# Kernel optimization log

Hardware: AMD Instinct MI355X
Metric: run time of the kernel (lower is better)

Reference implementation:

```python
import jax, jax.numpy as jnp
import numpy as np

ALPHA = 2.0   # surrogate.atan(alpha=2)
BETA = 0.9    # membrane decay
THR = 1.0     # spike threshold

@jax.custom_vjp
def atan_spike(x):
    # Heaviside forward, atan surrogate backward (snntorch convention)
    return (x > 0).astype(x.dtype)

def _atan_fwd(x):
    return atan_spike(x), x

def _atan_bwd(x, g):
    return (g * (ALPHA / 2.0) / (1.0 + (jnp.pi / 2.0 * ALPHA * x) ** 2),)

atan_spike.defvjp(_atan_fwd, _atan_bwd)


def setup_inputs() -> dict:
    key = jax.random.key(0)
    ks = jax.random.split(key, 7)
    B, T, I = 128, 128, 1024
    dims = [2048, 2048, 1024]
    x = jax.random.normal(ks[0], (B, T, I), dtype=jnp.float32)
    fan_ins = [I, dims[0], dims[1]]
    W0 = jax.random.normal(ks[1], (dims[0], fan_ins[0]), dtype=jnp.float32) / np.sqrt(fan_ins[0])
    b0 = jax.random.normal(ks[2], (dims[0],), dtype=jnp.float32) * 0.01
    W1 = jax.random.normal(ks[3], (dims[1], fan_ins[1]), dtype=jnp.float32) / np.sqrt(fan_ins[1])
    b1 = jax.random.normal(ks[4], (dims[1],), dtype=jnp.float32) * 0.01
    W2 = jax.random.normal(ks[5], (dims[2], fan_ins[2]), dtype=jnp.float32) / np.sqrt(fan_ins[2])
    b2 = jax.random.normal(ks[6], (dims[2],), dtype=jnp.float32) * 0.01
    return {"x": x, "W0": W0, "b0": b0, "W1": W1, "b1": b1, "W2": W2, "b2": b2}


def reference(x, W0, b0, W1, b1, W2, b2):
    params = ((W0, b0), (W1, b1), (W2, b2))
    B = x.shape[0]
    dims = [W0.shape[0], W1.shape[0], W2.shape[0]]
    v0 = tuple(jnp.zeros((B, d), x.dtype) for d in dims)

    def step(volts, x_t):
        h = x_t
        new_volts = []
        v = None
        for (W, b), vi in zip(params, volts):
            cur = h @ W.T + b            # [B, d]
            v = BETA * vi + cur           # leaky integration
            spk = atan_spike(v - THR)     # threshold
            v = v - spk * THR             # reset by subtraction
            new_volts.append(v)
            h = spk
        return tuple(new_volts), (h, v)

    xT = jnp.swapaxes(x, 0, 1)            # [T, B, I]
    _, (spikes, volts) = jax.lax.scan(step, v0, xT)
    # [T, B, D] -> [B, T, D]
    return jnp.swapaxes(spikes, 0, 1), jnp.swapaxes(volts, 0, 1)
```

## Files before the change

kernel.cpp:

```cpp
#include <hip/hip_runtime.h>
#include <stdint.h>


#define TT   128
#define NB   128
#define DD2  1024

#define SPK0_OFF 0u
#define SPK1_OFF (128u*128u*64u)
#define PART_OFF (2u*128u*128u*64u)
#define NHELP    96u
#define FLG_OFF  (PART_OFF + NHELP*8192u)
#define NFLG     1536u
#define WS_NEED_BYTES ((size_t)(FLG_OFF + NFLG) * 4u)

__device__ __forceinline__ void wait_ge(uint32_t* p, uint32_t tgt){
  while (__hip_atomic_load(p, __ATOMIC_ACQUIRE, __HIP_MEMORY_SCOPE_AGENT) < tgt)
    __builtin_amdgcn_s_sleep(1);
}

__device__ __forceinline__ constexpr int fswz(int k){
  return (k & 16) | ((k ^ (k >> 3)) & 12);
}

__global__ void sentinel_kernel(float* o){ o[0] = 42.0f; }

__global__ __launch_bounds__(512, 2) void snn_kernel(
    const float* __restrict__ x,
    const float* __restrict__ W0, const float* __restrict__ b0,
    const float* __restrict__ W1, const float* __restrict__ b1,
    const float* __restrict__ W2, const float* __restrict__ b2,
    float* __restrict__ out, uint32_t* __restrict__ ws)
{
  __shared__ __align__(16) float lA[2][128][68];
  __shared__ __align__(16) float lB[2][64][132];
  __shared__ uint32_t lBits[128];

  const int tid  = threadIdx.x;
  const int h    = tid >> 8;
  const int t256 = tid & 255;
  const int tm   = t256 & 15;
  const int tn   = t256 >> 4;
  const int bid  = blockIdx.x;

  uint32_t* spikes0  = ws + SPK0_OFF;
  uint32_t* spikes1  = ws + SPK1_OFF;
  float*    partials = (float*)(ws + PART_OFF);
  uint32_t* flg   = ws + FLG_OFF;
  uint32_t* pflag = flg;
  uint32_t* oflag = flg + 512;
  uint32_t* done0 = flg + 1024;
  uint32_t* done1 = flg + 1280;

  int group, pairk, tl, m0, n0, K, hslot;
  const float *Wl, *bl;
  const uint32_t* spkIn; uint32_t* spkOut;
  uint32_t *dIn, *dOut;
  if (bid < 64) {
    group=0; pairk=0; tl=bid;
    m0=(tl>>5)*64; n0=(tl&31)*64; K=1024; Wl=W0; bl=b0;
    spkIn=nullptr; spkOut=spikes0; dIn=nullptr; dOut=done0+(m0>>6)*128; hslot=-1;
  } else if (bid < 192) {
    group=1; int rel=bid-64; pairk=rel&1; tl=rel>>1;
    m0=(tl>>5)*64; n0=(tl&31)*64; K=2048; Wl=W1; bl=b1;
    spkIn=spikes0; spkOut=spikes1;
    dIn=done0+(m0>>6)*128; dOut=done1+(m0>>6)*128; hslot=tl;
  } else {
    group=2; int rel=bid-192; pairk=rel&1; tl=rel>>1;
    m0=(tl>>4)*64; n0=(tl&15)*64; K=2048; Wl=W2; bl=b2;
    spkIn=spikes1; spkOut=nullptr;
    dIn=done1+(m0>>6)*128; dOut=nullptr; hslot=64+tl;
  }
  const bool helper = (pairk == 1);
  const int  K0     = (pairk*2 + h)*512;

  float bias[4];
  #pragma unroll
  for (int c = 0; c < 4; ++c) bias[c] = bl[n0 + tn*4 + c];

  float vst[4][4];
  #pragma unroll
  for (int r = 0; r < 4; ++r)
    #pragma unroll
    for (int c = 0; c < 4; ++c) vst[r][c] = 0.f;

  const int e_mq   = t256 & 15;
  const int e_sub  = t256 >> 4;
  const int e_wsub = e_sub & 3;
  const int e_kq8  = e_sub >> 2;
  const int e_kloc = e_wsub*32 + e_kq8*8;

  float (*cA)[68]  = lA[h];
  float (*cB)[132] = lB[h];
  float* ex = &lA[1][0][0];

  for (int t = 0; t < TT; ++t) {
    if (dIn) {
      if (tid == 0) wait_ge(&dIn[t], 32u);
      __syncthreads();
    }

    float acc[4][4];
    #pragma unroll
    for (int r = 0; r < 4; ++r)
      #pragma unroll
      for (int c = 0; c < 4; ++c) acc[r][c] = 0.f;

    #pragma unroll 1
    for (int ch = 0; ch < 4; ++ch) {
      const int kb = K0 + ch*128;

      #pragma unroll
      for (int it = 0; it < 8; ++it) {
        int idx = t256 + it*256;
        int nrow = idx >> 5, kq = idx & 31;
        float4 w = *(const float4*)(Wl + (size_t)(n0+nrow)*K + kb + kq*4);
        *(float4*)&cB[nrow][kq*4] = w;
      }

      if (group == 0) {
        #pragma unroll
        for (int it = 0; it < 8; ++it) {
          int idx = t256 + it*256;
          int mrow = idx >> 5, kq = idx & 31;
          float4 v = *(const float4*)(x + ((size_t)(m0+mrow)*TT + t)*1024 + kb + kq*4);
          int k0 = kq*4;
          const int sw = fswz(k0);
          const int col = mrow ^ sw;
          cA[k0+0][col] = v.x; cA[k0+1][col] = v.y;
          cA[k0+2][col] = v.z; cA[k0+3][col] = v.w;
        }
      } else {
        const size_t rbase = ((size_t)t*NB + m0 + e_mq*4)*64 + (kb>>5) + e_wsub;
        uint32_t w0 = __hip_atomic_load(&spkIn[rbase      ], __ATOMIC_RELAXED, __HIP_MEMORY_SCOPE_AGENT);
        uint32_t w1 = __hip_atomic_load(&spkIn[rbase +  64], __ATOMIC_RELAXED, __HIP_MEMORY_SCOPE_AGENT);
        uint32_t w2 = __hip_atomic_load(&spkIn[rbase + 128], __ATOMIC_RELAXED, __HIP_MEMORY_SCOPE_AGENT);
        uint32_t w3 = __hip_atomic_load(&spkIn[rbase + 192], __ATOMIC_RELAXED, __HIP_MEMORY_SCOPE_AGENT);
        #pragma unroll
        for (int i = 0; i < 8; ++i) {
          int k  = e_kloc + i;
          int sh = k & 31;
          float4 f;
          f.x = ((w0 >> sh) & 1u) ? 1.0f : 0.0f;
          f.y = ((w1 >> sh) & 1u) ? 1.0f : 0.0f;
          f.z = ((w2 >> sh) & 1u) ? 1.0f : 0.0f;
          f.w = ((w3 >> sh) & 1u) ? 1.0f : 0.0f;
          *(float4*)&cA[k][(e_mq*4) ^ fswz(k)] = f;
        }
      }
      __syncthreads();

      #pragma unroll 4
      for (int k4 = 0; k4 < 32; ++k4) {
        const int kbase = k4*4;
        const int sw = fswz(kbase);
        const float* pa = &cA[kbase][(tm*4) ^ sw];
        const float4 q0 = *(const float4*)&cB[tn*4+0][kbase];
        const float4 q1 = *(const float4*)&cB[tn*4+1][kbase];
        const float4 q2 = *(const float4*)&cB[tn*4+2][kbase];
        const float4 q3 = *(const float4*)&cB[tn*4+3][kbase];
        #pragma unroll
        for (int u = 0; u < 4; ++u) {
          const float4 a  = *(const float4*)(pa + u*68);
          const float b0v = (u==0) ? q0.x : (u==1) ? q0.y : (u==2) ? q0.z : q0.w;
          const float b1v = (u==0) ? q1.x : (u==1) ? q1.y : (u==2) ? q1.z : q1.w;
          const float b2v = (u==0) ? q2.x : (u==1) ? q2.y : (u==2) ? q2.z : q2.w;
          const float b3v = (u==0) ? q3.x : (u==1) ? q3.y : (u==2) ? q3.z : q3.w;
          acc[0][0] = __builtin_fmaf(a.x, b0v, acc[0][0]);
          acc[1][0] = __builtin_fmaf(a.y, b0v, acc[1][0]);
          acc[2][0] = __builtin_fmaf(a.z, b0v, acc[2][0]);
          acc[3][0] = __builtin_fmaf(a.w, b0v, acc[3][0]);
          acc[0][1] = __builtin_fmaf(a.x, b1v, acc[0][1]);
          acc[1][1] = __builtin_fmaf(a.y, b1v, acc[1][1]);
          acc[2][1] = __builtin_fmaf(a.z, b1v, acc[2][1]);
          acc[3][1] = __builtin_fmaf(a.w, b1v, acc[3][1]);
          acc[0][2] = __builtin_fmaf(a.x, b2v, acc[0][2]);
          acc[1][2] = __builtin_fmaf(a.y, b2v, acc[1][2]);
          acc[2][2] = __builtin_fmaf(a.z, b2v, acc[2][2]);
          acc[3][2] = __builtin_fmaf(a.w, b2v, acc[3][2]);
          acc[0][3] = __builtin_fmaf(a.x, b3v, acc[0][3]);
          acc[1][3] = __builtin_fmaf(a.y, b3v, acc[1][3]);
          acc[2][3] = __builtin_fmaf(a.z, b3v, acc[2][3]);
          acc[3][3] = __builtin_fmaf(a.w, b3v, acc[3][3]);
        }
      }
      __syncthreads();
    }

    if (helper) {
      if (t >= 1) { if (tid == 0) wait_ge(&oflag[bid-1], (uint32_t)t); __syncthreads(); }
      uint64_t* pb = (uint64_t*)(partials + (size_t)hslot*8192 + (size_t)h*4096) + t256*8;
      #pragma unroll
      for (int r = 0; r < 4; ++r)
        #pragma unroll
        for (int cq = 0; cq < 2; ++cq) {
          union { float f[2]; uint64_t u; } cv;
          cv.f[0] = acc[r][cq*2+0]; cv.f[1] = acc[r][cq*2+1];
          __hip_atomic_store(&pb[r*2+cq], cv.u, __ATOMIC_RELAXED, __HIP_MEMORY_SCOPE_AGENT);
        }
      __syncthreads();
      if (tid == 0) __hip_atomic_store(&pflag[bid], (uint32_t)(t+1), __ATOMIC_RELEASE, __HIP_MEMORY_SCOPE_AGENT);
      continue;
    }

    if (h == 1) {
      #pragma unroll
      for (int r = 0; r < 4; ++r)
        *(float4*)&ex[t256*16 + r*4] = make_float4(acc[r][0], acc[r][1], acc[r][2], acc[r][3]);
    }
    __syncthreads();
    if (h == 0) {
      #pragma unroll
      for (int r = 0; r < 4; ++r)
        #pragma unroll
        for (int c = 0; c < 4; ++c)
          acc[r][c] = __fadd_rn(acc[r][c], ex[t256*16 + r*4 + c]);
    }

    if (group != 0) {
      if (tid == 0) wait_ge(&pflag[bid+1], (uint32_t)(t+1));
      __syncthreads();
      if (h == 0) {
        uint64_t* p2 = (uint64_t*)(partials + (size_t)hslot*8192) + t256*8;
        uint64_t* p3 = (uint64_t*)(partials + (size_t)hslot*8192 + 4096) + t256*8;
        #pragma unroll
        for (int r = 0; r < 4; ++r)
          #pragma unroll
          for (int cq = 0; cq < 2; ++cq) {
            union { uint64_t u; float f[2]; } cv;
            cv.u = __hip_atomic_load(&p2[r*2+cq], __ATOMIC_RELAXED, __HIP_MEMORY_SCOPE_AGENT);
            acc[r][cq*2+0] = __fadd_rn(acc[r][cq*2+0], cv.f[0]);
            acc[r][cq*2+1] = __fadd_rn(acc[r][cq*2+1], cv.f[1]);
          }
        #pragma unroll
        for (int r = 0; r < 4; ++r)
          #pragma unroll
          for (int cq = 0; cq < 2; ++cq) {
            union { uint64_t u; float f[2]; } cv;
            cv.u = __hip_atomic_load(&p3[r*2+cq], __ATOMIC_RELAXED, __HIP_MEMORY_SCOPE_AGENT);
            acc[r][cq*2+0] = __fadd_rn(acc[r][cq*2+0], cv.f[0]);
            acc[r][cq*2+1] = __fadd_rn(acc[r][cq*2+1], cv.f[1]);
          }
      }
      __syncthreads();
      if (tid == 0) __hip_atomic_store(&oflag[bid], (uint32_t)(t+1), __ATOMIC_RELEASE, __HIP_MEMORY_SCOPE_AGENT);
    }

    if (group < 2) { if (tid < 128) lBits[tid] = 0; __syncthreads(); }

    if (h == 0) {
      float sv[4][4], vv8[4][4];
      #pragma unroll
      for (int r = 0; r < 4; ++r) {
        uint32_t msk = 0;
        #pragma unroll
        for (int c = 0; c < 4; ++c) {
          float cur = __fadd_rn(acc[r][c], bias[c]);
          float vv  = __fadd_rn(__fmul_rn(0.9f, vst[r][c]), cur);
          float s   = (vv > 1.0f) ? 1.0f : 0.0f;
          vv = __fsub_rn(vv, s);
          vst[r][c] = vv;
          sv[r][c] = s; vv8[r][c] = vv;
          msk |= (s != 0.f) ? (1u << c) : 0u;
        }
        if (group < 2 && msk)
          atomicOr(&lBits[(tm*4 + r)*2 + (tn>>3)], msk << ((tn&7)*4));
      }
      if (group == 2) {
        #pragma unroll
        for (int r = 0; r < 4; ++r) {
          size_t o  = ((size_t)(m0 + tm*4 + r)*TT + t)*DD2 + n0 + tn*4;
          *(float4*)(out + o)  = make_float4(sv[r][0], sv[r][1], sv[r][2], sv[r][3]);
          size_t ov = (size_t)NB*TT*DD2 + o;
          *(float4*)(out + ov) = make_float4(vv8[r][0], vv8[r][1], vv8[r][2], vv8[r][3]);
        }
      }
    }

    if (group < 2) {
      __syncthreads();
      if (tid < 128)
        __hip_atomic_store(&spkOut[((size_t)t*NB + m0 + (tid>>1))*64 + (n0>>5) + (tid&1)],
                           lBits[tid], __ATOMIC_RELAXED, __HIP_MEMORY_SCOPE_AGENT);
      __syncthreads();
      if (tid == 0) __hip_atomic_fetch_add(&dOut[t], 1u, __ATOMIC_RELEASE, __HIP_MEMORY_SCOPE_AGENT);
    }
  }
}

extern "C" void kernel_launch(void* const* d_in, const int* in_sizes, int n_in,
                              void* d_out, int out_size, void* d_ws, size_t ws_size,
                              hipStream_t stream) {
  (void)in_sizes; (void)n_in; (void)out_size;
  float* outf = (float*)d_out;
  if (ws_size < WS_NEED_BYTES) {
    sentinel_kernel<<<1, 1, 0, stream>>>(outf);
    return;
  }
  const float* x  = (const float*)d_in[0];
  const float* W0 = (const float*)d_in[1];
  const float* b0 = (const float*)d_in[2];
  const float* W1 = (const float*)d_in[3];
  const float* b1 = (const float*)d_in[4];
  const float* W2 = (const float*)d_in[5];
  const float* b2 = (const float*)d_in[6];
  uint32_t* ws = (uint32_t*)d_ws;

  hipMemsetAsync(ws + FLG_OFF, 0, NFLG * sizeof(uint32_t), stream);

  snn_kernel<<<256, 512, 0, stream>>>(x, W0, b0, W1, b1, W2, b2, outf, ws);
}
```

Before: 6.312 ms.

## Prefetch next K-chunk into registers while computing current chunk

Restructures the per-timestep chunk loop into a software pipeline. Global loads of weights, x or spike bits for chunk ch+1 are issued into registers before the FMA loop over chunk ch runs, then written to LDS at the top of the next iteration. This is meant to hide global-memory latency behind compute, at the cost of extra live registers (about 16 float4 plus 4 words), which may reduce occupancy. The inner FMA loop unroll also goes from 4 to 8.

```diff
diff --git a/kernel.cpp b/kernel.cpp
--- a/kernel.cpp
+++ b/kernel.cpp
@@ -84,6 +84,9 @@
     #pragma unroll
     for (int c = 0; c < 4; ++c) vst[r][c] = 0.f;
 
+  const int s_kq4 = (t256 & 31) * 4;
+  const int s_r0  = t256 >> 5;
+
   const int e_mq   = t256 & 15;
   const int e_sub  = t256 >> 4;
   const int e_wsub = e_sub & 3;
@@ -94,6 +97,57 @@
   float (*cB)[132] = lB[h];
   float* ex = &lA[1][0][0];
 
+  float4   pb_[8];
+  float4   pa_[8];
+  uint32_t pw_[4];
+
+#define ISSUE(CH) do {                                                         \
+    const int kb_ = K0 + (CH)*128;                                             \
+    const float* gb_ = Wl + (size_t)(n0 + s_r0)*K + kb_ + s_kq4;               \
+    _Pragma("unroll")                                                          \
+    for (int it = 0; it < 8; ++it)                                             \
+      pb_[it] = *(const float4*)(gb_ + (size_t)it*8*K);                        \
+    if (group == 0) {                                                          \
+      const float* ga_ = x + ((size_t)(m0 + s_r0)*TT + t)*1024 + kb_ + s_kq4;  \
+      _Pragma("unroll")                                                        \
+      for (int it = 0; it < 8; ++it)                                           \
+        pa_[it] = *(const float4*)(ga_ + (size_t)it*8*TT*1024);                \
+    } else {                                                                   \
+      const size_t rb_ = ((size_t)t*NB + m0 + e_mq*4)*64 + (kb_>>5) + e_wsub;  \
+      _Pragma("unroll")                                                        \
+      for (int j = 0; j < 4; ++j)                                              \
+        pw_[j] = __hip_atomic_load(&spkIn[rb_ + (size_t)j*64],                 \
+                                   __ATOMIC_RELAXED, __HIP_MEMORY_SCOPE_AGENT);\
+    }                                                                          \
+  } while (0)
+
+#define WRITE_LDS() do {                                                       \
+    _Pragma("unroll")                                                          \
+    for (int it = 0; it < 8; ++it)                                             \
+      *(float4*)&cB[s_r0 + it*8][s_kq4] = pb_[it];                             \
+    if (group == 0) {                                                          \
+      const int k0_ = s_kq4, sw_ = fswz(k0_);                                  \
+      _Pragma("unroll")                                                        \
+      for (int it = 0; it < 8; ++it) {                                         \
+        const int col = (s_r0 + it*8) ^ sw_;                                   \
+        cA[k0_+0][col] = pa_[it].x; cA[k0_+1][col] = pa_[it].y;                \
+        cA[k0_+2][col] = pa_[it].z; cA[k0_+3][col] = pa_[it].w;                \
+      }                                                                        \
+    } else {                                                                   \
+      _Pragma("unroll")                                                        \
+      for (int i = 0; i < 8; ++i) {                                            \
+        const int k_ = e_kloc + i;                                             \
+        const int sh_ = k_ & 31;                                               \
+        float4 f_;                                                             \
+        f_.x = ((pw_[0] >> sh_) & 1u) ? 1.0f : 0.0f;                           \
+        f_.y = ((pw_[1] >> sh_) & 1u) ? 1.0f : 0.0f;                           \
+        f_.z = ((pw_[2] >> sh_) & 1u) ? 1.0f : 0.0f;                           \
+        f_.w = ((pw_[3] >> sh_) & 1u) ? 1.0f : 0.0f;                           \
+        *(float4*)&cA[k_][(e_mq*4) ^ fswz(k_)] = f_;                           \
+      }                                                                        \
+    }                                                                          \
+  } while (0)
+
   for (int t = 0; t < TT; ++t) {
     if (dIn) {
       if (tid == 0) wait_ge(&dIn[t], 32u);
@@ -106,51 +160,15 @@
       #pragma unroll
       for (int c = 0; c < 4; ++c) acc[r][c] = 0.f;
 
+    ISSUE(0);
+
     #pragma unroll 1
     for (int ch = 0; ch < 4; ++ch) {
-      const int kb = K0 + ch*128;
-
-      #pragma unroll
-      for (int it = 0; it < 8; ++it) {
-        int idx = t256 + it*256;
-        int nrow = idx >> 5, kq = idx & 31;
-        float4 w = *(const float4*)(Wl + (size_t)(n0+nrow)*K + kb + kq*4);
-        *(float4*)&cB[nrow][kq*4] = w;
-      }
-
-      if (group == 0) {
-        #pragma unroll
-        for (int it = 0; it < 8; ++it) {
-          int idx = t256 + it*256;
-          int mrow = idx >> 5, kq = idx & 31;
-          float4 v = *(const float4*)(x + ((size_t)(m0+mrow)*TT + t)*1024 + kb + kq*4);
-          int k0 = kq*4;
-          const int sw = fswz(k0);
-          const int col = mrow ^ sw;
-          cA[k0+0][col] = v.x; cA[k0+1][col] = v.y;
-          cA[k0+2][col] = v.z; cA[k0+3][col] = v.w;
-        }
-      } else {
-        const size_t rbase = ((size_t)t*NB + m0 + e_mq*4)*64 + (kb>>5) + e_wsub;
-        uint32_t w0 = __hip_atomic_load(&spkIn[rbase      ], __ATOMIC_RELAXED, __HIP_MEMORY_SCOPE_AGENT);
-        uint32_t w1 = __hip_atomic_load(&spkIn[rbase +  64], __ATOMIC_RELAXED, __HIP_MEMORY_SCOPE_AGENT);
-        uint32_t w2 = __hip_atomic_load(&spkIn[rbase + 128], __ATOMIC_RELAXED, __HIP_MEMORY_SCOPE_AGENT);
-        uint32_t w3 = __hip_atomic_load(&spkIn[rbase + 192], __ATOMIC_RELAXED, __HIP_MEMORY_SCOPE_AGENT);
-        #pragma unroll
-        for (int i = 0; i < 8; ++i) {
-          int k  = e_kloc + i;
-          int sh = k & 31;
-          float4 f;
-          f.x = ((w0 >> sh) & 1u) ? 1.0f : 0.0f;
-          f.y = ((w1 >> sh) & 1u) ? 1.0f : 0.0f;
-          f.z = ((w2 >> sh) & 1u) ? 1.0f : 0.0f;
-          f.w = ((w3 >> sh) & 1u) ? 1.0f : 0.0f;
-          *(float4*)&cA[k][(e_mq*4) ^ fswz(k)] = f;
-        }
-      }
-      __syncthreads();
-
-      #pragma unroll 4
+      WRITE_LDS();
+      __syncthreads();
+      if (ch < 3) ISSUE(ch+1);
+
+      #pragma unroll 8
       for (int k4 = 0; k4 < 32; ++k4) {
         const int kbase = k4*4;
         const int sw = fswz(kbase);
@@ -286,6 +304,8 @@
       if (tid == 0) __hip_atomic_fetch_add(&dOut[t], 1u, __ATOMIC_RELEASE, __HIP_MEMORY_SCOPE_AGENT);
     }
   }
+#undef ISSUE
+#undef WRITE_LDS
 }
 
 extern "C" void kernel_launch(void* const* d_in, const int* in_sizes, int n_in,
```

After: 8.672 ms. 37.4% more time.

## Batch four timesteps per GEMM pass to reuse weight tiles across time

Applied to the files above, without the earlier changes.

Each block now computes the input GEMM for four consecutive timesteps at once, loading each weight K-chunk into shared memory once and reusing it for all four. The K chunk shrinks from 128 to 32 and the activation tile gains a time dimension. The aim is to cut repeated weight traffic and per-step sync overhead. The cost is 64 accumulator registers per thread, which pressures occupancy. Downstream layers must also wait for four steps of upstream spikes before starting, which coarsens inter-layer pipelining.

```diff
diff --git a/kernel.cpp b/kernel.cpp
--- a/kernel.cpp
+++ b/kernel.cpp
@@ -32,8 +32,8 @@
     const float* __restrict__ W2, const float* __restrict__ b2,
     float* __restrict__ out, uint32_t* __restrict__ ws)
 {
-  __shared__ __align__(16) float lA[2][128][68];
-  __shared__ __align__(16) float lB[2][64][132];
+  __shared__ __align__(16) float lA[2][4][32][68];
+  __shared__ __align__(16) float lB[2][64][36];
   __shared__ uint32_t lBits[128];
 
   const int tid  = threadIdx.x;
@@ -84,206 +84,222 @@
     #pragma unroll
     for (int c = 0; c < 4; ++c) vst[r][c] = 0.f;
 
-  const int e_mq   = t256 & 15;
-  const int e_sub  = t256 >> 4;
-  const int e_wsub = e_sub & 3;
-  const int e_kq8  = e_sub >> 2;
-  const int e_kloc = e_wsub*32 + e_kq8*8;
-
-  float (*cA)[68]  = lA[h];
-  float (*cB)[132] = lB[h];
-  float* ex = &lA[1][0][0];
-
-  for (int t = 0; t < TT; ++t) {
+  const int e_row = t256 >> 2;
+  const int e_g2  = (t256 & 3) * 2;
+
+  float (*cA)[32][68] = lA[h];
+  float (*cB)[36]     = lB[h];
+  float* ex = &lA[1][0][0][0];
+
+  for (int t4 = 0; t4 < TT; t4 += 4) {
     if (dIn) {
-      if (tid == 0) wait_ge(&dIn[t], 32u);
+      if (tid == 0) {
+        wait_ge(&dIn[t4+0], 32u); wait_ge(&dIn[t4+1], 32u);
+        wait_ge(&dIn[t4+2], 32u); wait_ge(&dIn[t4+3], 32u);
+      }
       __syncthreads();
     }
 
-    float acc[4][4];
+    float acc[4][4][4];
     #pragma unroll
-    for (int r = 0; r < 4; ++r)
+    for (int tt = 0; tt < 4; ++tt)
       #pragma unroll
-      for (int c = 0; c < 4; ++c) acc[r][c] = 0.f;
+      for (int r = 0; r < 4; ++r)
+        #pragma unroll
+        for (int c = 0; c < 4; ++c) acc[tt][r][c] = 0.f;
 
     #pragma unroll 1
-    for (int ch = 0; ch < 4; ++ch) {
-      const int kb = K0 + ch*128;
+    for (int ch = 0; ch < 16; ++ch) {
+      const int kb = K0 + ch*32;
 
       #pragma unroll
-      for (int it = 0; it < 8; ++it) {
+      for (int it = 0; it < 2; ++it) {
         int idx = t256 + it*256;
-        int nrow = idx >> 5, kq = idx & 31;
+        int nrow = idx >> 3, kq = idx & 7;
         float4 w = *(const float4*)(Wl + (size_t)(n0+nrow)*K + kb + kq*4);
         *(float4*)&cB[nrow][kq*4] = w;
       }
 
       if (group == 0) {
         #pragma unroll
-        for (int it = 0; it < 8; ++it) {
-          int idx = t256 + it*256;
-          int mrow = idx >> 5, kq = idx & 31;
-          float4 v = *(const float4*)(x + ((size_t)(m0+mrow)*TT + t)*1024 + kb + kq*4);
-          int k0 = kq*4;
-          const int sw = fswz(k0);
-          const int col = mrow ^ sw;
-          cA[k0+0][col] = v.x; cA[k0+1][col] = v.y;
-          cA[k0+2][col] = v.z; cA[k0+3][col] = v.w;
-        }
+        for (int tt = 0; tt < 4; ++tt)
+          #pragma unroll
+          for (int it = 0; it < 2; ++it) {
+            int idx = t256 + it*256;
+            int mrow = idx >> 3, kq = idx & 7;
+            float4 v = *(const float4*)(x + ((size_t)(m0+mrow)*TT + (t4+tt))*1024 + kb + kq*4);
+            const int k0 = kq*4;
+            const int col = mrow ^ fswz(k0);
+            cA[tt][k0+0][col] = v.x; cA[tt][k0+1][col] = v.y;
+            cA[tt][k0+2][col] = v.z; cA[tt][k0+3][col] = v.w;
+          }
       } else {
-        const size_t rbase = ((size_t)t*NB + m0 + e_mq*4)*64 + (kb>>5) + e_wsub;
-        uint32_t w0 = __hip_atomic_load(&spkIn[rbase      ], __ATOMIC_RELAXED, __HIP_MEMORY_SCOPE_AGENT);
-        uint32_t w1 = __hip_atomic_load(&spkIn[rbase +  64], __ATOMIC_RELAXED, __HIP_MEMORY_SCOPE_AGENT);
-        uint32_t w2 = __hip_atomic_load(&spkIn[rbase + 128], __ATOMIC_RELAXED, __HIP_MEMORY_SCOPE_AGENT);
-        uint32_t w3 = __hip_atomic_load(&spkIn[rbase + 192], __ATOMIC_RELAXED, __HIP_MEMORY_SCOPE_AGENT);
-        #pragma unroll
-        for (int i = 0; i < 8; ++i) {
-          int k  = e_kloc + i;
-          int sh = k & 31;
-          float4 f;
-          f.x = ((w0 >> sh) & 1u) ? 1.0f : 0.0f;
-          f.y = ((w1 >> sh) & 1u) ? 1.0f : 0.0f;
-          f.z = ((w2 >> sh) & 1u) ? 1.0f : 0.0f;
-          f.w = ((w3 >> sh) & 1u) ? 1.0f : 0.0f;
-          *(float4*)&cA[k][(e_mq*4) ^ fswz(k)] = f;
+        #pragma unroll
+        for (int tt = 0; tt < 4; ++tt) {
+          uint32_t w = __hip_atomic_load(
+              &spkIn[((size_t)(t4+tt)*NB + m0 + e_row)*64 + (kb>>5)],
+              __ATOMIC_RELAXED, __HIP_MEMORY_SCOPE_AGENT);
+          #pragma unroll
+          for (int gq = 0; gq < 2; ++gq) {
+            const int k0  = (e_g2 + gq)*4;
+            const int col = e_row ^ fswz(k0);
+            cA[tt][k0+0][col] = ((w >> (k0+0)) & 1u) ? 1.0f : 0.0f;
+            cA[tt][k0+1][col] = ((w >> (k0+1)) & 1u) ? 1.0f : 0.0f;
+            cA[tt][k0+2][col] = ((w >> (k0+2)) & 1u) ? 1.0f : 0.0f;
+            cA[tt][k0+3][col] = ((w >> (k0+3)) & 1u) ? 1.0f : 0.0f;
+          }
         }
       }
       __syncthreads();
 
-      #pragma unroll 4
-      for (int k4 = 0; k4 < 32; ++k4) {
-        const int kbase = k4*4;
-        const int sw = fswz(kbase);
-        const float* pa = &cA[kbase][(tm*4) ^ sw];
-        const float4 q0 = *(const float4*)&cB[tn*4+0][kbase];
-        const float4 q1 = *(const float4*)&cB[tn*4+1][kbase];
-        const float4 q2 = *(const float4*)&cB[tn*4+2][kbase];
-        const float4 q3 = *(const float4*)&cB[tn*4+3][kbase];
+      #pragma unroll 2
+      for (int k4 = 0; k4 < 8; ++k4) {
+        const int kb4 = k4*4;
+        const int sw  = fswz(kb4);
+        const int qa  = (tm*4) ^ sw;
+        const float4 q0 = *(const float4*)&cB[tn*4+0][kb4];
+        const float4 q1 = *(const float4*)&cB[tn*4+1][kb4];
+        const float4 q2 = *(const float4*)&cB[tn*4+2][kb4];
+        const float4 q3 = *(const float4*)&cB[tn*4+3][kb4];
         #pragma unroll
         for (int u = 0; u < 4; ++u) {
-          const float4 a  = *(const float4*)(pa + u*68);
           const float b0v = (u==0) ? q0.x : (u==1) ? q0.y : (u==2) ? q0.z : q0.w;
           const float b1v = (u==0) ? q1.x : (u==1) ? q1.y : (u==2) ? q1.z : q1.w;
           const float b2v = (u==0) ? q2.x : (u==1) ? q2.y : (u==2) ? q2.z : q2.w;
           const float b3v = (u==0) ? q3.x : (u==1) ? q3.y : (u==2) ? q3.z : q3.w;
-          acc[0][0] = __builtin_fmaf(a.x, b0v, acc[0][0]);
-          acc[1][0] = __builtin_fmaf(a.y, b0v, acc[1][0]);
-          acc[2][0] = __builtin_fmaf(a.z, b0v, acc[2][0]);
-          acc[3][0] = __builtin_fmaf(a.w, b0v, acc[3][0]);
-          acc[0][1] = __builtin_fmaf(a.x, b1v, acc[0][1]);
-          acc[1][1] = __builtin_fmaf(a.y, b1v, acc[1][1]);
-          acc[2][1] = __builtin_fmaf(a.z, b1v, acc[2][1]);
-          acc[3][1] = __builtin_fmaf(a.w, b1v, acc[3][1]);
-          acc[0][2] = __builtin_fmaf(a.x, b2v, acc[0][2]);
-          acc[1][2] = __builtin_fmaf(a.y, b2v, acc[1][2]);
-          acc[2][2] = __builtin_fmaf(a.z, b2v, acc[2][2]);
-          acc[3][2] = __builtin_fmaf(a.w, b2v, acc[3][2]);
-          acc[0][3] = __builtin_fmaf(a.x, b3v, acc[0][3]);
-          acc[1][3] = __builtin_fmaf(a.y, b3v, acc[1][3]);
-          acc[2][3] = __builtin_fmaf(a.z, b3v, acc[2][3]);
-          acc[3][3] = __builtin_fmaf(a.w, b3v, acc[3][3]);
+          #pragma unroll
+          for (int tt = 0; tt < 4; ++tt) {
+            const float4 a = *(const float4*)&cA[tt][kb4+u][qa];
+            acc[tt][0][0] = __builtin_fmaf(a.x, b0v, acc[tt][0][0]);
+            acc[tt][1][0] = __builtin_fmaf(a.y, b0v, acc[tt][1][0]);
+            acc[tt][2][0] = __builtin_fmaf(a.z, b0v, acc[tt][2][0]);
+            acc[tt][3][0] = __builtin_fmaf(a.w, b0v, acc[tt][3][0]);
+            acc[tt][0][1] = __builtin_fmaf(a.x, b1v, acc[tt][0][1]);
+            acc[tt][1][1] = __builtin_fmaf(a.y, b1v, acc[tt][1][1]);
+            acc[tt][2][1] = __builtin_fmaf(a.z, b1v, acc[tt][2][1]);
+            acc[tt][3][1] = __builtin_fmaf(a.w, b1v, acc[tt][3][1]);
+            acc[tt][0][2] = __builtin_fmaf(a.x, b2v, acc[tt][0][2]);
+            acc[tt][1][2] = __builtin_fmaf(a.y, b2v, acc[tt][1][2]);
+            acc[tt][2][2] = __builtin_fmaf(a.z, b2v, acc[tt][2][2]);
+            acc[tt][3][2] = __builtin_fmaf(a.w, b2v, acc[tt][3][2]);
+            acc[tt][0][3] = __builtin_fmaf(a.x, b3v, acc[tt][0][3]);
+            acc[tt][1][3] = __builtin_fmaf(a.y, b3v, acc[tt][1][3]);
+            acc[tt][2][3] = __builtin_fmaf(a.z, b3v, acc[tt][2][3]);
+            acc[tt][3][3] = __builtin_fmaf(a.w, b3v, acc[tt][3][3]);
+          }
         }
       }
       __syncthreads();
     }
 
     if (helper) {
-      if (t >= 1) { if (tid == 0) wait_ge(&oflag[bid-1], (uint32_t)t); __syncthreads(); }
-      uint64_t* pb = (uint64_t*)(partials + (size_t)hslot*8192 + (size_t)h*4096) + t256*8;
       #pragma unroll
-      for (int r = 0; r < 4; ++r)
-        #pragma unroll
-        for (int cq = 0; cq < 2; ++cq) {
-          union { float f[2]; uint64_t u; } cv;
-          cv.f[0] = acc[r][cq*2+0]; cv.f[1] = acc[r][cq*2+1];
-          __hip_atomic_store(&pb[r*2+cq], cv.u, __ATOMIC_RELAXED, __HIP_MEMORY_SCOPE_AGENT);
-        }
-      __syncthreads();
-      if (tid == 0) __hip_atomic_store(&pflag[bid], (uint32_t)(t+1), __ATOMIC_RELEASE, __HIP_MEMORY_SCOPE_AGENT);
+      for (int tt = 0; tt < 4; ++tt) {
+        const int gt = t4 + tt;
+        if (gt >= 1) { if (tid == 0) wait_ge(&oflag[bid-1], (uint32_t)gt); __syncthreads(); }
+        uint64_t* pb = (uint64_t*)(partials + (size_t)hslot*8192 + (size_t)h*4096) + t256*8;
+        #pragma unroll
+        for (int r = 0; r < 4; ++r)
+          #pragma unroll
+          for (int cq = 0; cq < 2; ++cq) {
+            union { float f[2]; uint64_t u; } cv;
+            cv.f[0] = acc[tt][r][cq*2+0]; cv.f[1] = acc[tt][r][cq*2+1];
+            __hip_atomic_store(&pb[r*2+cq], cv.u, __ATOMIC_RELAXED, __HIP_MEMORY_SCOPE_AGENT);
+          }
+        __syncthreads();
+        if (tid == 0) __hip_atomic_store(&pflag[bid], (uint32_t)(gt+1), __ATOMIC_RELEASE, __HIP_MEMORY_SCOPE_AGENT);
+      }
       continue;
     }
 
-    if (h == 1) {
-      #pragma unroll
-      for (int r = 0; r < 4; ++r)
-        *(float4*)&ex[t256*16 + r*4] = make_float4(acc[r][0], acc[r][1], acc[r][2], acc[r][3]);
-    }
-    __syncthreads();
-    if (h == 0) {
-      #pragma unroll
-      for (int r = 0; r < 4; ++r)
-        #pragma unroll
-        for (int c = 0; c < 4; ++c)
-          acc[r][c] = __fadd_rn(acc[r][c], ex[t256*16 + r*4 + c]);
-    }
-
-    if (group != 0) {
-      if (tid == 0) wait_ge(&pflag[bid+1], (uint32_t)(t+1));
+    #pragma unroll
+    for (int tt = 0; tt < 4; ++tt) {
+      const int gt = t4 + tt;
+
+      if (h == 1) {
+        #pragma unroll
+        for (int r = 0; r < 4; ++r)
+          *(float4*)&ex[t256*16 + r*4] =
+              make_float4(acc[tt][r][0], acc[tt][r][1], acc[tt][r][2], acc[tt][r][3]);
+      }
       __syncthreads();
+      float mg[4][4];
       if (h == 0) {
-        uint64_t* p2 = (uint64_t*)(partials + (size_t)hslot*8192) + t256*8;
-        uint64_t* p3 = (uint64_t*)(partials + (size_t)hslot*8192 + 4096) + t256*8;
         #pragma unroll
         for (int r = 0; r < 4; ++r)
           #pragma unroll
-          for (int cq = 0; cq < 2; ++cq) {
-            union { uint64_t u; float f[2]; } cv;
-            cv.u = __hip_atomic_load(&p2[r*2+cq], __ATOMIC_RELAXED, __HIP_MEMORY_SCOPE_AGENT);
-            acc[r][cq*2+0] = __fadd_rn(acc[r][cq*2+0], cv.f[0]);
-            acc[r][cq*2+1] = __fadd_rn(acc[r][cq*2+1], cv.f[1]);
-          }
-        #pragma unroll
-        for (int r = 0; r < 4; ++r)
-          #pragma unroll
-          for (int cq = 0; cq < 2; ++cq) {
-            union { uint64_t u; float f[2]; } cv;
-            cv.u = __hip_atomic_load(&p3[r*2+cq], __ATOMIC_RELAXED, __HIP_MEMORY_SCOPE_AGENT);
-            acc[r][cq*2+0] = __fadd_rn(acc[r][cq*2+0], cv.f[0]);
-            acc[r][cq*2+1] = __fadd_rn(acc[r][cq*2+1], cv.f[1]);
-          }
-      }
-      __syncthreads();
-      if (tid == 0) __hip_atomic_store(&oflag[bid], (uint32_t)(t+1), __ATOMIC_RELEASE, __HIP_MEMORY_SCOPE_AGENT);
-    }
-
-    if (group < 2) { if (tid < 128) lBits[tid] = 0; __syncthreads(); }
-
-    if (h == 0) {
-      float sv[4][4], vv8[4][4];
-      #pragma unroll
-      for (int r = 0; r < 4; ++r) {
-        uint32_t msk = 0;
-        #pragma unroll
-        for (int c = 0; c < 4; ++c) {
-          float cur = __fadd_rn(acc[r][c], bias[c]);
-          float vv  = __fadd_rn(__fmul_rn(0.9f, vst[r][c]), cur);
-          float s   = (vv > 1.0f) ? 1.0f : 0.0f;
-          vv = __fsub_rn(vv, s);
-          vst[r][c] = vv;
-          sv[r][c] = s; vv8[r][c] = vv;
-          msk |= (s != 0.f) ? (1u << c) : 0u;
-        }
-        if (group < 2 && msk)
-          atomicOr(&lBits[(tm*4 + r)*2 + (tn>>3)], msk << ((tn&7)*4));
-      }
-      if (group == 2) {
+          for (int c = 0; c < 4; ++c)
+            mg[r][c] = __fadd_rn(acc[tt][r][c], ex[t256*16 + r*4 + c]);
+      }
+
+      if (group != 0) {
+        if (tid == 0) wait_ge(&pflag[bid+1], (uint32_t)(gt+1));
+        __syncthreads();
+        if (h == 0) {
+          uint64_t* p2 = (uint64_t*)(partials + (size_t)hslot*8192) + t256*8;
+          uint64_t* p3 = (uint64_t*)(partials + (size_t)hslot*8192 + 4096) + t256*8;
+          #pragma unroll
+          for (int r = 0; r < 4; ++r)
+            #pragma unroll
+            for (int cq = 0; cq < 2; ++cq) {
+              union { uint64_t u; float f[2]; } cv;
+              cv.u = __hip_atomic_load(&p2[r*2+cq], __ATOMIC_RELAXED, __HIP_MEMORY_SCOPE_AGENT);
+              mg[r][cq*2+0] = __fadd_rn(mg[r][cq*2+0], cv.f[0]);
+              mg[r][cq*2+1] = __fadd_rn(mg[r][cq*2+1], cv.f[1]);
+            }
+          #pragma unroll
+          for (int r = 0; r < 4; ++r)
+            #pragma unroll
+            for (int cq = 0; cq < 2; ++cq) {
+              union { uint64_t u; float f[2]; } cv;
+              cv.u = __hip_atomic_load(&p3[r*2+cq], __ATOMIC_RELAXED, __HIP_MEMORY_SCOPE_AGENT);
+              mg[r][cq*2+0] = __fadd_rn(mg[r][cq*2+0], cv.f[0]);
+              mg[r][cq*2+1] = __fadd_rn(mg[r][cq*2+1], cv.f[1]);
+            }
+        }
+        __syncthreads();
+        if (tid == 0) __hip_atomic_store(&oflag[bid], (uint32_t)(gt+1), __ATOMIC_RELEASE, __HIP_MEMORY_SCOPE_AGENT);
+      }
+
+      if (group < 2) { if (tid < 128) lBits[tid] = 0; __syncthreads(); }
+
+      if (h == 0) {
+        float sv[4][4], vv8[4][4];
         #pragma unroll
         for (int r = 0; r < 4; ++r) {
-          size_t o  = ((size_t)(m0 + tm*4 + r)*TT + t)*DD2 + n0 + tn*4;
-          *(float4*)(out + o)  = make_float4(sv[r][0], sv[r][1], sv[r][2], sv[r][3]);
-          size_t ov = (size_t)NB*TT*DD2 + o;
-          *(float4*)(out + ov) = make_float4(vv8[r][0], vv8[r][1], vv8[r][2], vv8[r][3]);
-        }
-      }
-    }
-
-    if (group < 2) {
-      __syncthreads();
-      if (tid < 128)
-        __hip_atomic_store(&spkOut[((size_t)t*NB + m0 + (tid>>1))*64 + (n0>>5) + (tid&1)],
-                           lBits[tid], __ATOMIC_RELAXED, __HIP_MEMORY_SCOPE_AGENT);
-      __syncthreads();
-      if (tid == 0) __hip_atomic_fetch_add(&dOut[t], 1u, __ATOMIC_RELEASE, __HIP_MEMORY_SCOPE_AGENT);
+          uint32_t msk = 0;
+          #pragma unroll
+          for (int c = 0; c < 4; ++c) {
+            float cur = __fadd_rn(mg[r][c], bias[c]);
+            float vv  = __fadd_rn(__fmul_rn(0.9f, vst[r][c]), cur);
+            float s   = (vv > 1.0f) ? 1.0f : 0.0f;
+            vv = __fsub_rn(vv, s);
+            vst[r][c] = vv;
+            sv[r][c] = s; vv8[r][c] = vv;
+            msk |= (s != 0.f) ? (1u << c) : 0u;
+          }
+          if (group < 2 && msk)
+            atomicOr(&lBits[(tm*4 + r)*2 + (tn>>3)], msk << ((tn&7)*4));
+        }
+        if (group == 2) {
+          #pragma unroll
+          for (int r = 0; r < 4; ++r) {
+            size_t o  = ((size_t)(m0 + tm*4 + r)*TT + gt)*DD2 + n0 + tn*4;
+            *(float4*)(out + o)  = make_float4(sv[r][0], sv[r][1], sv[r][2], sv[r][3]);
+            size_t ov = (size_t)NB*TT*DD2 + o;
+            *(float4*)(out + ov) = make_float4(vv8[r][0], vv8[r][1], vv8[r][2], vv8[r][3]);
+          }
+        }
+      }
+
+      if (group < 2) {
+        __syncthreads();
+        if (tid < 128)
+          __hip_atomic_store(&spkOut[((size_t)gt*NB + m0 + (tid>>1))*64 + (n0>>5) + (tid&1)],
+                             lBits[tid], __ATOMIC_RELAXED, __HIP_MEMORY_SCOPE_AGENT);
+        __syncthreads();
+        if (tid == 0) __hip_atomic_fetch_add(&dOut[gt], 1u, __ATOMIC_RELEASE, __HIP_MEMORY_SCOPE_AGENT);
+      }
     }
   }
 }
```

New measurement: 7.480 ms. +18.5%, slower.
